# Optimization experiments

Measured on AMD Instinct MI355X. Metric: run time of the kernel, lower is better.

Reference implementation:

```python
import jax, jax.numpy as jnp
import numpy as np

N_HEAD = 16
N_EMBD = 1024
BLOCK = 2048
B, T = 4, 2048


def setup_inputs() -> dict:
    key = jax.random.key(0)
    ks = jax.random.split(key, 5)
    s = 0.02
    return {
        "x": jax.random.normal(ks[0], (B, T, N_EMBD), dtype=jnp.float32),
        "qkv_w": jax.random.normal(ks[1], (3 * N_EMBD, N_EMBD), dtype=jnp.float32) * s,
        "qkv_b": jnp.zeros((3 * N_EMBD,), dtype=jnp.float32),
        "proj_w": jax.random.normal(ks[2], (N_EMBD, N_EMBD), dtype=jnp.float32) * s,
        "proj_b": jnp.zeros((N_EMBD,), dtype=jnp.float32),
    }


def reference(x, qkv_w, qkv_b, proj_w, proj_b):
    Bx, Tx, C = x.shape
    hd = C // N_HEAD
    qkv = x @ qkv_w.T + qkv_b  # [B,T,3C]
    q, k, v = jnp.split(qkv, 3, axis=-1)
    # [B,T,C] -> [B,H,T,hd]
    def heads(t):
        return t.reshape(Bx, Tx, N_HEAD, hd).transpose(0, 2, 1, 3)
    q, k, v = heads(q), heads(k), heads(v)
    scores = jnp.einsum("bhqd,bhkd->bhqk", q, k) / jnp.sqrt(jnp.float32(hd))
    causal = jnp.tril(jnp.ones((Tx, Tx), dtype=bool))
    scores = jnp.where(causal[None, None, :, :], scores, -jnp.inf)
    attn = jax.nn.softmax(scores, axis=-1)
    out = jnp.einsum("bhqk,bhkd->bhqd", attn, v)
    out = out.transpose(0, 2, 1, 3).reshape(Bx, Tx, C)
    return out @ proj_w.T + proj_b
```

## Files before the change

### kernel.cpp

```cpp
#include <hip/hip_runtime.h>
#include <stdint.h>
#include <math.h>

#define DEVI __device__ __forceinline__

typedef __attribute__((ext_vector_type(8))) short bf16x8;
typedef __attribute__((ext_vector_type(4))) float f32x4;

DEVI unsigned short f2bf(float f) {
  union { float f; unsigned u; } v; v.f = f;
  unsigned u = v.u;
  u += 0x7fffu + ((u >> 16) & 1u);
  return (unsigned short)(u >> 16);
}

DEVI unsigned cvt_pk_bf16(float a, float b) {
  unsigned r;
  asm("v_cvt_pk_bf16_f32 %0, %1, %2" : "=v"(r) : "v"(a), "v"(b));
  return r;
}

DEVI f32x4 mfma16(bf16x8 a, bf16x8 b, f32x4 c) {
  return __builtin_amdgcn_mfma_f32_16x16x32_bf16(a, b, c, 0, 0, 0);
}

DEVI void gld16(const unsigned short* g, unsigned short* l) {
  __builtin_amdgcn_global_load_lds(
      (const __attribute__((address_space(1))) unsigned int*)(uintptr_t)g,
      (__attribute__((address_space(3))) unsigned int*)(unsigned int)(uintptr_t)l,
      16, 0, 0);
}

#define VMCNT(n) asm volatile("s_waitcnt vmcnt(" #n ")" ::: "memory")
#define BAR()                              \
  do {                                     \
    __builtin_amdgcn_s_barrier();          \
    __builtin_amdgcn_sched_barrier(0);     \
  } while (0)

template <int N> DEVI void vmcntc() {
  static_assert(N >= 0 && N <= 8, "");
  if constexpr (N == 0) VMCNT(0);
  else if constexpr (N == 2) VMCNT(2);
  else if constexpr (N == 3) VMCNT(3);
  else if constexpr (N == 4) VMCNT(4);
}

__global__ __launch_bounds__(256) void cvt3_kernel(
    const float* __restrict__ a, unsigned short* __restrict__ oa,
    const float* __restrict__ b, unsigned short* __restrict__ ob,
    const float* __restrict__ c, unsigned short* __restrict__ oc) {
  int bid = blockIdx.x;
  const float* in; unsigned short* out; int i;
  if (bid < 8192)       { in = a; out = oa; i = bid; }
  else if (bid < 11264) { in = b; out = ob; i = bid - 8192; }
  else                  { in = c; out = oc; i = bid - 11264; }
  int idx = (i * 256 + (int)threadIdx.x) * 4;
  float4 v = *(const float4*)(in + idx);
  unsigned lo = f2bf(v.x) | ((unsigned)f2bf(v.y) << 16);
  unsigned hi = f2bf(v.z) | ((unsigned)f2bf(v.w) << 16);
  uint2 o; o.x = lo; o.y = hi;
  *(uint2*)(out + idx) = o;
}

template <int MODE, int NTA, int NTB>
__global__ __launch_bounds__(512, 2) void gemm8(
    const unsigned short* __restrict__ A, const unsigned short* __restrict__ Bw,
    const float* __restrict__ bias, float* __restrict__ Cf,
    unsigned short* __restrict__ Qo, unsigned short* __restrict__ Ko,
    unsigned short* __restrict__ Vo, int M, int N, int K, int nbx) {
  constexpr int NTT = NTA + NTB;
  constexpr int WTN = NTT * 16;
  constexpr int BN = 4 * WTN;
  constexpr int B_USH = BN * 64;
  constexpr int BUFS = 16384 + B_USH;
  extern __shared__ unsigned short lds[];
  const int tid = threadIdx.x;
  const int lane = tid & 63;
  const int w = tid >> 6;
  const int wm = w >> 2, wn = w & 3;
  const int lr = lane & 15, lq = lane >> 4;

  const int cpx = gridDim.x >> 3;
  const int swz = (blockIdx.x & 7) * cpx + (blockIdx.x >> 3);
  const int bx = swz % nbx, by = swz / nbx;
  const int m0 = by * 256, n0 = bx * BN;

  const int sr = lane >> 3;
  const int sc = ((lane & 7) ^ sr) << 3;
  const unsigned short* pa = A + (size_t)(m0 + sr) * K + sc;
  const unsigned short* pb = Bw + (size_t)(n0 + sr) * K + sc;

  const int bs0 = (lq ^ (lr & 7)) << 3;
  const int bs1 = ((lq + 4) ^ (lr & 7)) << 3;

  f32x4 acc[8][NTT] = {};

  auto sA = [&](int buf, int kt, int c) {
    gld16(pa + (size_t)(c << 3) * K + kt, lds + buf * BUFS + (c << 9));
  };
  auto sB = [&](int buf, int kt, int c) {
    gld16(pb + (size_t)(c << 3) * K + kt, lds + buf * BUFS + 16384 + (c << 9));
  };
  auto sAa = [&](int buf, int kt) { sA(buf, kt, w); sA(buf, kt, 16 + w); };
  auto sAb = [&](int buf, int kt) { sA(buf, kt, 8 + w); sA(buf, kt, 24 + w); };
  auto sBa = [&](int buf, int kt) {
#pragma unroll
    for (int k2 = 0; k2 < NTA; ++k2)
      sB(buf, kt, (w & 3) * NTT * 2 + (w >> 2) * NTA + k2);
  };
  auto sBb = [&](int buf, int kt) {
#pragma unroll
    for (int k2 = 0; k2 < NTB; ++k2)
      sB(buf, kt, (w & 3) * NTT * 2 + NTA * 2 + (w >> 2) * NTB + k2);
  };

#define LDA(A_, mh)                                                          \
  _Pragma("unroll") for (int i = 0; i < 4; ++i) {                            \
    int ar = wm * 128 + (mh) * 64 + i * 16 + lr;                             \
    A_[i][0] = *(const bf16x8*)(As_ + ar * 64 + bs0);                        \
    A_[i][1] = *(const bf16x8*)(As_ + ar * 64 + bs1);                        \
  }
#define LDB(B_, CNT, ntb)                                                    \
  _Pragma("unroll") for (int j = 0; j < (CNT); ++j) {                        \
    int br = wn * WTN + ((ntb) + j) * 16 + lr;                               \
    B_[j][0] = *(const bf16x8*)(Bs_ + br * 64 + bs0);                        \
    B_[j][1] = *(const bf16x8*)(Bs_ + br * 64 + bs1);                        \
  }
#define MM(A_, B_, mh, CNT, ntb)                                             \
  __builtin_amdgcn_s_setprio(1);                                             \
  _Pragma("unroll") for (int i = 0; i < 4; ++i)                              \
    _Pragma("unroll") for (int j = 0; j < (CNT); ++j) {                      \
      acc[(mh) * 4 + i][(ntb) + j] =                                         \
          mfma16(A_[i][0], B_[j][0], acc[(mh) * 4 + i][(ntb) + j]);          \
      acc[(mh) * 4 + i][(ntb) + j] =                                         \
          mfma16(A_[i][1], B_[j][1], acc[(mh) * 4 + i][(ntb) + j]);          \
    }                                                                        \
  __builtin_amdgcn_s_setprio(0);

  sAa(0, 0); sBa(0, 0); sBb(0, 0); sAb(0, 0);
  vmcntc<NTB + 2>();
  BAR();

  const int NT = K >> 6;
  for (int t = 0; t < NT - 1; ++t) {
    const int buf = t & 1, nb = buf ^ 1;
    const int kt = (t + 1) << 6;
    const unsigned short* As_ = lds + buf * BUFS;
    const unsigned short* Bs_ = As_ + 16384;
    bf16x8 af[4][2], baf[NTA][2], bbf[NTB][2];
    sAa(nb, kt);
    LDA(af, 0); LDB(baf, NTA, 0);
    MM(af, baf, 0, NTA, 0);
    vmcntc<4>(); BAR();
    sBa(nb, kt);
    LDB(bbf, NTB, NTA);
    MM(af, bbf, 0, NTB, NTA);
    vmcntc<NTA + 2>(); BAR();
    sBb(nb, kt);
    LDA(af, 1);
    MM(af, bbf, 1, NTB, NTA);
    sAb(nb, kt);
    MM(af, baf, 1, NTA, 0);
    vmcntc<NTB + 2>(); BAR();
  }
  {
    const int buf = (NT - 1) & 1;
    const unsigned short* As_ = lds + buf * BUFS;
    const unsigned short* Bs_ = As_ + 16384;
    bf16x8 af[4][2], baf[NTA][2], bbf[NTB][2];
    LDA(af, 0); LDB(baf, NTA, 0);
    MM(af, baf, 0, NTA, 0);
    vmcntc<2>(); BAR();
    LDB(bbf, NTB, NTA);
    MM(af, bbf, 0, NTB, NTA);
    vmcntc<0>(); BAR();
    LDA(af, 1);
    MM(af, bbf, 1, NTB, NTA);
    MM(af, baf, 1, NTA, 0);
  }
#undef LDA
#undef LDB
#undef MM

#pragma unroll
  for (int mt = 0; mt < 8; ++mt) {
#pragma unroll
    for (int nt = 0; nt < NTT; ++nt) {
      int n_g = n0 + wn * WTN + nt * 16 + lr;
      float bv = bias[n_g];
      if (MODE == 1) {
#pragma unroll
        for (int r = 0; r < 4; ++r) {
          int m_g = m0 + wm * 128 + mt * 16 + lq * 4 + r;
          Cf[(size_t)m_g * N + n_g] = acc[mt][nt][r] + bv;
        }
      } else {
        int which = n_g >> 10;
        int rem = n_g & 1023;
        int h = rem >> 6, d = rem & 63;
        int m_base = m0 + wm * 128 + mt * 16 + lq * 4;
        int b = m_base >> 11, tt = m_base & 2047;
        if (which == 2) {
          uint2 pv;
          pv.x = cvt_pk_bf16(acc[mt][nt][0] + bv, acc[mt][nt][1] + bv);
          pv.y = cvt_pk_bf16(acc[mt][nt][2] + bv, acc[mt][nt][3] + bv);
          *(uint2*)(Vo + (((size_t)(b * 16 + h) * 64 + d) * 2048 + tt)) = pv;
        } else {
          unsigned short* p = (which == 0) ? Qo : Ko;
#pragma unroll
          for (int r = 0; r < 4; ++r) {
            size_t idx = (((size_t)(b * 16 + h) * 2048) + tt + r) * 64 + d;
            p[idx] = f2bf(acc[mt][nt][r] + bv);
          }
        }
      }
    }
  }
}

__global__ __launch_bounds__(512, 2) void attn_kernel(
    const unsigned short* __restrict__ Q, const unsigned short* __restrict__ K,
    const unsigned short* __restrict__ V, unsigned short* __restrict__ Y) {
  constexpr int T = 2048, HD = 64, H = 16;
  __shared__ unsigned short Kt[2][64 * 72];
  __shared__ unsigned short Vt[2][64 * 72];
  __shared__ unsigned short Pt[8][16 * 68];

  const int tid = threadIdx.x;
  const int lane = tid & 63;
  const int w = tid >> 6;
  const int lr = lane & 15, lq = lane >> 4;
  const int pair = blockIdx.x;
  const int h = blockIdx.y;
  const int b = blockIdx.z;
  const size_t bh = (size_t)(b * H + h) * T * HD;
  const float SC = 0.125f * 1.44269504089f;

  const int krow = tid >> 3, kcb = (tid & 7) << 3;

  float4 kr, vr;
  auto load_tile = [&](int jt) {
    const int c0 = jt * 64;
    kr = *(const float4*)(K + bh + (size_t)(c0 + krow) * HD + kcb);
    vr = *(const float4*)(V + bh + (size_t)krow * T + c0 + kcb);
  };
  auto stage = [&](int buf) {
    *(float4*)(&Kt[buf][krow * 72 + kcb]) = kr;
    *(float4*)(&Vt[buf][krow * 72 + kcb]) = vr;
  };

  load_tile(0);

  for (int phase = 0; phase < 2; ++phase) {
    const int qt = phase ? (7 - pair) : pair;
    const int q0 = qt * 256;
    const int nkv = 4 * (qt + 1);
    const int qw = q0 + w * 32;

    bf16x8 qf[2][2];
#pragma unroll
    for (int qs = 0; qs < 2; ++qs)
#pragma unroll
      for (int kb = 0; kb < 2; ++kb)
        qf[qs][kb] = *(const bf16x8*)(Q + bh + (size_t)(qw + qs * 16 + lr) * HD +
                                      kb * 32 + lq * 8);

    f32x4 o[2][4] = {};
    float mi[2] = {-INFINITY, -INFINITY}, li[2] = {0.f, 0.f};

    stage(0);
    load_tile(1);
    __syncthreads();

    for (int jt = 0; jt < nkv; ++jt) {
      const int c0 = jt * 64;
      const int buf = jt & 1;

      if (c0 <= qw + 31) {
        f32x4 s[2][4];
        __builtin_amdgcn_s_setprio(1);
#pragma unroll
        for (int nt = 0; nt < 4; ++nt) {
          bf16x8 kf0 = *(const bf16x8*)(&Kt[buf][(nt * 16 + lr) * 72 + lq * 8]);
          bf16x8 kf1 = *(const bf16x8*)(&Kt[buf][(nt * 16 + lr) * 72 + 32 + lq * 8]);
#pragma unroll
          for (int qs = 0; qs < 2; ++qs) {
            f32x4 z = {};
            z = mfma16(kf0, qf[qs][0], z);
            s[qs][nt] = mfma16(kf1, qf[qs][1], z);
          }
        }
        __builtin_amdgcn_s_setprio(0);
        if (c0 + 63 > qw) {
#pragma unroll
          for (int qs = 0; qs < 2; ++qs) {
            int qg = qw + qs * 16 + lr;
#pragma unroll
            for (int nt = 0; nt < 4; ++nt)
#pragma unroll
              for (int r = 0; r < 4; ++r) {
                int kvg = c0 + nt * 16 + lq * 4 + r;
                if (kvg > qg) s[qs][nt][r] = -INFINITY;
              }
          }
        }
        float mxs[2];
#pragma unroll
        for (int qs = 0; qs < 2; ++qs) {
          float mx = -INFINITY;
#pragma unroll
          for (int nt = 0; nt < 4; ++nt)
            mx = fmaxf(mx, fmaxf(fmaxf(s[qs][nt][0], s[qs][nt][1]),
                                 fmaxf(s[qs][nt][2], s[qs][nt][3])));
          mx = fmaxf(mx, __shfl_xor(mx, 16));
          mx = fmaxf(mx, __shfl_xor(mx, 32));
          mxs[qs] = mx * SC;
        }
        if (!__all((mxs[0] <= mi[0] + 8.f) && (mxs[1] <= mi[1] + 8.f))) {
#pragma unroll
          for (int qs = 0; qs < 2; ++qs) {
            float mnew = fmaxf(mi[qs], mxs[qs]);
            float alpha = __builtin_amdgcn_exp2f(mi[qs] - mnew);
            mi[qs] = mnew;
            li[qs] *= alpha;
#pragma unroll
            for (int nt = 0; nt < 4; ++nt)
#pragma unroll
              for (int r = 0; r < 4; ++r) o[qs][nt][r] *= alpha;
          }
        }
        bf16x8 pf[2][2];
#pragma unroll
        for (int qs = 0; qs < 2; ++qs) {
          float rs = 0.f;
#pragma unroll
          for (int nt = 0; nt < 4; ++nt) {
            float p0 = __builtin_amdgcn_exp2f(fmaf(s[qs][nt][0], SC, -mi[qs]));
            float p1 = __builtin_amdgcn_exp2f(fmaf(s[qs][nt][1], SC, -mi[qs]));
            float p2 = __builtin_amdgcn_exp2f(fmaf(s[qs][nt][2], SC, -mi[qs]));
            float p3 = __builtin_amdgcn_exp2f(fmaf(s[qs][nt][3], SC, -mi[qs]));
            rs += (p0 + p1) + (p2 + p3);
            uint2 pk;
            pk.x = cvt_pk_bf16(p0, p1);
            pk.y = cvt_pk_bf16(p2, p3);
            *(uint2*)(&Pt[w][lr * 68 + nt * 16 + lq * 4]) = pk;
          }
          li[qs] += rs;
#pragma unroll
          for (int kb = 0; kb < 2; ++kb) {
            union { uint2 u[2]; bf16x8 v; } pu;
            pu.u[0] = *(const uint2*)(&Pt[w][lr * 68 + kb * 32 + lq * 8]);
            __builtin_amdgcn_sched_barrier(0);
            pu.u[1] = *(const uint2*)(&Pt[w][lr * 68 + kb * 32 + lq * 8 + 4]);
            pf[qs][kb] = pu.v;
          }
        }
        __builtin_amdgcn_s_setprio(1);
#pragma unroll
        for (int nt = 0; nt < 4; ++nt) {
          bf16x8 vf0 = *(const bf16x8*)(&Vt[buf][(nt * 16 + lr) * 72 + lq * 8]);
          bf16x8 vf1 = *(const bf16x8*)(&Vt[buf][(nt * 16 + lr) * 72 + 32 + lq * 8]);
#pragma unroll
          for (int qs = 0; qs < 2; ++qs) {
            o[qs][nt] = mfma16(vf0, pf[qs][0], o[qs][nt]);
            o[qs][nt] = mfma16(vf1, pf[qs][1], o[qs][nt]);
          }
        }
        __builtin_amdgcn_s_setprio(0);
      }

      if (jt + 1 < nkv) {
        stage(buf ^ 1);
        if (jt + 2 < nkv) load_tile(jt + 2);
        else if (phase == 0) load_tile(0);
        __syncthreads();
      }
    }

#pragma unroll
    for (int qs = 0; qs < 2; ++qs) {
      float l = li[qs];
      l += __shfl_xor(l, 16);
      l += __shfl_xor(l, 32);
      float inv = 1.f / l;
      int t_g = qw + qs * 16 + lr;
#pragma unroll
      for (int nt = 0; nt < 4; ++nt) {
        uint2 yv;
        yv.x = cvt_pk_bf16(o[qs][nt][0] * inv, o[qs][nt][1] * inv);
        yv.y = cvt_pk_bf16(o[qs][nt][2] * inv, o[qs][nt][3] * inv);
        *(uint2*)(Y + ((size_t)(b * T + t_g)) * 1024 + h * 64 + nt * 16 + lq * 4) = yv;
      }
    }
  }
}

extern "C" void kernel_launch(void* const* d_in, const int* in_sizes, int n_in,
                              void* d_out, int out_size, void* d_ws, size_t ws_size,
                              hipStream_t stream) {
  const float* x = (const float*)d_in[0];
  const float* qkv_w = (const float*)d_in[1];
  const float* qkv_b = (const float*)d_in[2];
  const float* proj_w = (const float*)d_in[3];
  const float* proj_b = (const float*)d_in[4];
  float* out = (float*)d_out;

  unsigned short* ws = (unsigned short*)d_ws;
  unsigned short* xb = ws;
  unsigned short* wqkv = xb + 8388608;
  unsigned short* wproj = wqkv + 3145728;
  unsigned short* Qb = wproj + 1048576;
  unsigned short* Kb = Qb + 8388608;
  unsigned short* Vb = Kb + 8388608;
  unsigned short* Yb = Vb + 8388608;

  auto* g0 = gemm8<0, 2, 1>;
  auto* g1 = gemm8<1, 1, 1>;
  static bool attr_set = false;
  if (!attr_set) {
    (void)hipFuncSetAttribute((const void*)g0,
                              hipFuncAttributeMaxDynamicSharedMemorySize, 114688);
    (void)hipFuncSetAttribute((const void*)g1,
                              hipFuncAttributeMaxDynamicSharedMemorySize, 98304);
    attr_set = true;
  }

  cvt3_kernel<<<12288, 256, 0, stream>>>(x, xb, qkv_w, wqkv, proj_w, wproj);

  gemm8<0, 2, 1><<<dim3(512), 512, 114688, stream>>>(xb, wqkv, qkv_b, nullptr, Qb,
                                                     Kb, Vb, 8192, 3072, 1024, 16);
  attn_kernel<<<dim3(4, 16, 4), 512, 0, stream>>>(Qb, Kb, Vb, Yb);
  gemm8<1, 1, 1><<<dim3(256), 512, 98304, stream>>>(Yb, wproj, proj_b, out, nullptr,
                                                    nullptr, nullptr, 8192, 1024,
                                                    1024, 8);
}
```

Measured before the change: 242.2 us.

## Software-pipeline attention loop: overlap next QK^T with current softmax/PV using triple buffers

Restructures the causal attention inner loop so the QK^T MFMAs for tile j+1 are issued before the softmax and PV of tile j, using two score register sets and a three-slot K/V shared-memory ring. The aim is to hide the softmax exp/max latency behind matrix-core work. It raises register pressure, since two score tiles are live at once, and LDS use, which could reduce occupancy at launch bounds (512,2). It also adds an extra barrier at each phase start.

```diff
diff --git a/kernel.cpp b/kernel.cpp
--- a/kernel.cpp
+++ b/kernel.cpp
@@ -223,8 +223,8 @@
     const unsigned short* __restrict__ Q, const unsigned short* __restrict__ K,
     const unsigned short* __restrict__ V, unsigned short* __restrict__ Y) {
   constexpr int T = 2048, HD = 64, H = 16;
-  __shared__ unsigned short Kt[2][64 * 72];
-  __shared__ unsigned short Vt[2][64 * 72];
+  __shared__ unsigned short Kt[3][64 * 72];
+  __shared__ unsigned short Vt[3][64 * 72];
   __shared__ unsigned short Pt[8][16 * 68];
 
   const int tid = threadIdx.x;
@@ -269,114 +269,128 @@
     f32x4 o[2][4] = {};
     float mi[2] = {-INFINITY, -INFINITY}, li[2] = {0.f, 0.f};
 
+    auto qkt = [&](f32x4 (&S_)[2][4], int j) {
+      if (j * 64 > qw + 31) return;
+      const unsigned short* Kb_ = Kt[j % 3];
+      __builtin_amdgcn_s_setprio(1);
+#pragma unroll
+      for (int nt = 0; nt < 4; ++nt) {
+        bf16x8 kf0 = *(const bf16x8*)(Kb_ + (nt * 16 + lr) * 72 + lq * 8);
+        bf16x8 kf1 = *(const bf16x8*)(Kb_ + (nt * 16 + lr) * 72 + 32 + lq * 8);
+#pragma unroll
+        for (int qs = 0; qs < 2; ++qs) {
+          f32x4 z = {};
+          z = mfma16(kf0, qf[qs][0], z);
+          S_[qs][nt] = mfma16(kf1, qf[qs][1], z);
+        }
+      }
+      __builtin_amdgcn_s_setprio(0);
+    };
+
+    auto finish = [&](f32x4 (&S_)[2][4], int jm) {
+      const int c0m = jm * 64;
+      if (c0m > qw + 31) return;
+      const unsigned short* Vb_ = Vt[jm % 3];
+      if (c0m + 63 > qw) {
+#pragma unroll
+        for (int qs = 0; qs < 2; ++qs) {
+          int qg = qw + qs * 16 + lr;
+#pragma unroll
+          for (int nt = 0; nt < 4; ++nt)
+#pragma unroll
+            for (int r = 0; r < 4; ++r) {
+              int kvg = c0m + nt * 16 + lq * 4 + r;
+              if (kvg > qg) S_[qs][nt][r] = -INFINITY;
+            }
+        }
+      }
+      float mxs[2];
+#pragma unroll
+      for (int qs = 0; qs < 2; ++qs) {
+        float mx = -INFINITY;
+#pragma unroll
+        for (int nt = 0; nt < 4; ++nt)
+          mx = fmaxf(mx, fmaxf(fmaxf(S_[qs][nt][0], S_[qs][nt][1]),
+                               fmaxf(S_[qs][nt][2], S_[qs][nt][3])));
+        mx = fmaxf(mx, __shfl_xor(mx, 16));
+        mx = fmaxf(mx, __shfl_xor(mx, 32));
+        mxs[qs] = mx * SC;
+      }
+      if (!__all((mxs[0] <= mi[0] + 8.f) && (mxs[1] <= mi[1] + 8.f))) {
+#pragma unroll
+        for (int qs = 0; qs < 2; ++qs) {
+          float mnew = fmaxf(mi[qs], mxs[qs]);
+          float alpha = __builtin_amdgcn_exp2f(mi[qs] - mnew);
+          mi[qs] = mnew;
+          li[qs] *= alpha;
+#pragma unroll
+          for (int nt = 0; nt < 4; ++nt)
+#pragma unroll
+            for (int r = 0; r < 4; ++r) o[qs][nt][r] *= alpha;
+        }
+      }
+      bf16x8 pf[2][2];
+#pragma unroll
+      for (int qs = 0; qs < 2; ++qs) {
+        float rs = 0.f;
+#pragma unroll
+        for (int nt = 0; nt < 4; ++nt) {
+          float p0 = __builtin_amdgcn_exp2f(fmaf(S_[qs][nt][0], SC, -mi[qs]));
+          float p1 = __builtin_amdgcn_exp2f(fmaf(S_[qs][nt][1], SC, -mi[qs]));
+          float p2 = __builtin_amdgcn_exp2f(fmaf(S_[qs][nt][2], SC, -mi[qs]));
+          float p3 = __builtin_amdgcn_exp2f(fmaf(S_[qs][nt][3], SC, -mi[qs]));
+          rs += (p0 + p1) + (p2 + p3);
+          uint2 pk;
+          pk.x = cvt_pk_bf16(p0, p1);
+          pk.y = cvt_pk_bf16(p2, p3);
+          *(uint2*)(&Pt[w][lr * 68 + nt * 16 + lq * 4]) = pk;
+        }
+        li[qs] += rs;
+#pragma unroll
+        for (int kb = 0; kb < 2; ++kb) {
+          union { uint2 u[2]; bf16x8 v; } pu;
+          pu.u[0] = *(const uint2*)(&Pt[w][lr * 68 + kb * 32 + lq * 8]);
+          __builtin_amdgcn_sched_barrier(0);
+          pu.u[1] = *(const uint2*)(&Pt[w][lr * 68 + kb * 32 + lq * 8 + 4]);
+          pf[qs][kb] = pu.v;
+        }
+      }
+      __builtin_amdgcn_s_setprio(1);
+#pragma unroll
+      for (int nt = 0; nt < 4; ++nt) {
+        bf16x8 vf0 = *(const bf16x8*)(Vb_ + (nt * 16 + lr) * 72 + lq * 8);
+        bf16x8 vf1 = *(const bf16x8*)(Vb_ + (nt * 16 + lr) * 72 + 32 + lq * 8);
+#pragma unroll
+        for (int qs = 0; qs < 2; ++qs) {
+          o[qs][nt] = mfma16(vf0, pf[qs][0], o[qs][nt]);
+          o[qs][nt] = mfma16(vf1, pf[qs][1], o[qs][nt]);
+        }
+      }
+      __builtin_amdgcn_s_setprio(0);
+    };
+
+    __syncthreads();
     stage(0);
     load_tile(1);
     __syncthreads();
 
-    for (int jt = 0; jt < nkv; ++jt) {
-      const int c0 = jt * 64;
-      const int buf = jt & 1;
-
-      if (c0 <= qw + 31) {
-        f32x4 s[2][4];
-        __builtin_amdgcn_s_setprio(1);
-#pragma unroll
-        for (int nt = 0; nt < 4; ++nt) {
-          bf16x8 kf0 = *(const bf16x8*)(&Kt[buf][(nt * 16 + lr) * 72 + lq * 8]);
-          bf16x8 kf1 = *(const bf16x8*)(&Kt[buf][(nt * 16 + lr) * 72 + 32 + lq * 8]);
-#pragma unroll
-          for (int qs = 0; qs < 2; ++qs) {
-            f32x4 z = {};
-            z = mfma16(kf0, qf[qs][0], z);
-            s[qs][nt] = mfma16(kf1, qf[qs][1], z);
-          }
-        }
-        __builtin_amdgcn_s_setprio(0);
-        if (c0 + 63 > qw) {
-#pragma unroll
-          for (int qs = 0; qs < 2; ++qs) {
-            int qg = qw + qs * 16 + lr;
-#pragma unroll
-            for (int nt = 0; nt < 4; ++nt)
-#pragma unroll
-              for (int r = 0; r < 4; ++r) {
-                int kvg = c0 + nt * 16 + lq * 4 + r;
-                if (kvg > qg) s[qs][nt][r] = -INFINITY;
-              }
-          }
-        }
-        float mxs[2];
-#pragma unroll
-        for (int qs = 0; qs < 2; ++qs) {
-          float mx = -INFINITY;
-#pragma unroll
-          for (int nt = 0; nt < 4; ++nt)
-            mx = fmaxf(mx, fmaxf(fmaxf(s[qs][nt][0], s[qs][nt][1]),
-                                 fmaxf(s[qs][nt][2], s[qs][nt][3])));
-          mx = fmaxf(mx, __shfl_xor(mx, 16));
-          mx = fmaxf(mx, __shfl_xor(mx, 32));
-          mxs[qs] = mx * SC;
-        }
-        if (!__all((mxs[0] <= mi[0] + 8.f) && (mxs[1] <= mi[1] + 8.f))) {
-#pragma unroll
-          for (int qs = 0; qs < 2; ++qs) {
-            float mnew = fmaxf(mi[qs], mxs[qs]);
-            float alpha = __builtin_amdgcn_exp2f(mi[qs] - mnew);
-            mi[qs] = mnew;
-            li[qs] *= alpha;
-#pragma unroll
-            for (int nt = 0; nt < 4; ++nt)
-#pragma unroll
-              for (int r = 0; r < 4; ++r) o[qs][nt][r] *= alpha;
-          }
-        }
-        bf16x8 pf[2][2];
-#pragma unroll
-        for (int qs = 0; qs < 2; ++qs) {
-          float rs = 0.f;
-#pragma unroll
-          for (int nt = 0; nt < 4; ++nt) {
-            float p0 = __builtin_amdgcn_exp2f(fmaf(s[qs][nt][0], SC, -mi[qs]));
-            float p1 = __builtin_amdgcn_exp2f(fmaf(s[qs][nt][1], SC, -mi[qs]));
-            float p2 = __builtin_amdgcn_exp2f(fmaf(s[qs][nt][2], SC, -mi[qs]));
-            float p3 = __builtin_amdgcn_exp2f(fmaf(s[qs][nt][3], SC, -mi[qs]));
-            rs += (p0 + p1) + (p2 + p3);
-            uint2 pk;
-            pk.x = cvt_pk_bf16(p0, p1);
-            pk.y = cvt_pk_bf16(p2, p3);
-            *(uint2*)(&Pt[w][lr * 68 + nt * 16 + lq * 4]) = pk;
-          }
-          li[qs] += rs;
-#pragma unroll
-          for (int kb = 0; kb < 2; ++kb) {
-            union { uint2 u[2]; bf16x8 v; } pu;
-            pu.u[0] = *(const uint2*)(&Pt[w][lr * 68 + kb * 32 + lq * 8]);
-            __builtin_amdgcn_sched_barrier(0);
-            pu.u[1] = *(const uint2*)(&Pt[w][lr * 68 + kb * 32 + lq * 8 + 4]);
-            pf[qs][kb] = pu.v;
-          }
-        }
-        __builtin_amdgcn_s_setprio(1);
-#pragma unroll
-        for (int nt = 0; nt < 4; ++nt) {
-          bf16x8 vf0 = *(const bf16x8*)(&Vt[buf][(nt * 16 + lr) * 72 + lq * 8]);
-          bf16x8 vf1 = *(const bf16x8*)(&Vt[buf][(nt * 16 + lr) * 72 + 32 + lq * 8]);
-#pragma unroll
-          for (int qs = 0; qs < 2; ++qs) {
-            o[qs][nt] = mfma16(vf0, pf[qs][0], o[qs][nt]);
-            o[qs][nt] = mfma16(vf1, pf[qs][1], o[qs][nt]);
-          }
-        }
-        __builtin_amdgcn_s_setprio(0);
-      }
-
-      if (jt + 1 < nkv) {
-        stage(buf ^ 1);
-        if (jt + 2 < nkv) load_tile(jt + 2);
-        else if (phase == 0) load_tile(0);
+    f32x4 sA[2][4], sB[2][4];
+    for (int j = 0; j < nkv; j += 2) {
+      qkt(sA, j);
+      if (j > 0) finish(sB, j - 1);
+      stage((j + 1) % 3);
+      if (j + 2 < nkv) load_tile(j + 2);
+      else if (phase == 0) load_tile(0);
+      __syncthreads();
+      qkt(sB, j + 1);
+      finish(sA, j);
+      if (j + 2 < nkv) {
+        stage((j + 2) % 3);
+        load_tile(j + 3);
         __syncthreads();
       }
     }
+    finish(sB, nkv - 1);
 
 #pragma unroll
     for (int qs = 0; qs < 2; ++qs) {
```

Measured after the change: 236.1 us. 2.5% less time.
